# Kernel tuning notes

Hardware: AMD Instinct MI355X
Metric: run time of the kernel (lower is better)

## Reference

```python
import jax, jax.numpy as jnp
import numpy as np

D_MODEL = 2048
NUM_Q_HEADS = 16
NUM_KV_HEADS = 4
HEAD_DIM = D_MODEL // NUM_Q_HEADS  # 128
NUM_GROUPS = NUM_Q_HEADS // NUM_KV_HEADS  # 4
ROPE_BASE = 10000.0


def _rope_cos_sin(seq_len, head_dim):
    inv_freq = 1.0 / (ROPE_BASE ** (jnp.arange(0, head_dim, 2, dtype=jnp.float32) / head_dim))
    t = jnp.arange(seq_len, dtype=jnp.float32)
    freqs = jnp.outer(t, inv_freq)            # [S, head_dim/2]
    emb = jnp.concatenate([freqs, freqs], -1)  # [S, head_dim]
    return jnp.cos(emb)[None, :, None, :], jnp.sin(emb)[None, :, None, :]


def _rotate_half(x):
    half = x.shape[-1] // 2
    return jnp.concatenate([-x[..., half:], x[..., :half]], axis=-1)


def setup_inputs() -> dict:
    key = jax.random.key(0)
    k0, k1, k2, k3, k4 = jax.random.split(key, 5)
    B, S = 2, 2048
    kv_dim = HEAD_DIM * NUM_KV_HEADS
    scale = D_MODEL ** -0.5
    return {
        "x": jax.random.normal(k0, (B, S, D_MODEL), jnp.float32),
        "attention_mask": jnp.ones((B, S), jnp.int32),
        "Wq": jax.random.normal(k1, (D_MODEL, D_MODEL), jnp.float32) * scale,
        "Wk": jax.random.normal(k2, (D_MODEL, kv_dim), jnp.float32) * scale,
        "Wv": jax.random.normal(k3, (D_MODEL, kv_dim), jnp.float32) * scale,
        "Wo": jax.random.normal(k4, (D_MODEL, D_MODEL), jnp.float32) * scale,
    }


def reference(x, attention_mask, Wq, Wk, Wv, Wo):
    B, S, _ = x.shape
    q = (x @ Wq).reshape(B, S, NUM_Q_HEADS, HEAD_DIM)
    k = (x @ Wk).reshape(B, S, NUM_KV_HEADS, HEAD_DIM)
    v = (x @ Wv).reshape(B, S, NUM_KV_HEADS, HEAD_DIM)

    cos, sin = _rope_cos_sin(S, HEAD_DIM)  # [1,S,1,hd]
    q = q * cos + _rotate_half(q) * sin
    k = k * cos + _rotate_half(k) * sin

    # [B, H, S, hd]; replicate KV heads across groups (repeat_interleave)
    q = q.transpose(0, 2, 1, 3)
    k = jnp.repeat(k.transpose(0, 2, 1, 3), NUM_GROUPS, axis=1)
    v = jnp.repeat(v.transpose(0, 2, 1, 3), NUM_GROUPS, axis=1)

    scale = HEAD_DIM ** -0.5
    scores = jnp.einsum("bhqd,bhkd->bhqk", q, k) * scale
    mask = attention_mask[:, None, None, :]  # [B,1,1,S] over keys
    scores = jnp.where(mask == 0, jnp.float32(-jnp.inf), scores)
    probs = jax.nn.softmax(scores, axis=-1)
    out = jnp.einsum("bhqk,bhkd->bhqd", probs, v)
    out = out.transpose(0, 2, 1, 3).reshape(B, S, D_MODEL)
    return out @ Wo
```

## Files before the change

### kernel.cpp

```cpp
#include <hip/hip_runtime.h>
#include <hip/hip_bf16.h>

typedef __attribute__((ext_vector_type(4))) float f32x4;
typedef __attribute__((ext_vector_type(16))) float f32x16;
typedef __attribute__((ext_vector_type(8))) short s16x8;
typedef __attribute__((ext_vector_type(4))) short s16x4;
typedef __attribute__((ext_vector_type(2))) unsigned int u32x2;

__device__ __forceinline__ float fexp2(float x) {
    float y; asm("v_exp_f32 %0, %1" : "=v"(y) : "v"(x)); return y;
}

__global__ void tables_prep(float* __restrict__ cosT, float* __restrict__ sinT,
                            const int* __restrict__ mask, float* __restrict__ mb) {
    const int bid = blockIdx.x;
    if (bid < 2048) {
        const int s = bid, j = threadIdx.x;
        const float inv = exp2f(-(float)j * (13.287712379549449f / 64.f));
        const float f = (float)s * inv;
        cosT[s * 64 + j] = cosf(f);
        sinT[s * 64 + j] = sinf(f);
    } else {
        const int base = (bid - 2048) * 64 + threadIdx.x;
#pragma unroll
        for (int k = 0; k < 4; ++k)
            mb[base + k * 1024] = (mask[base + k * 1024] == 0) ? -1e30f : 0.f;
    }
}

__global__ __launch_bounds__(256)
void cast_f32_bf16(const float* __restrict__ src, __hip_bfloat16* __restrict__ dst, int n4) {
    const int i = blockIdx.x * 256 + threadIdx.x;
    if (i < n4) {
        f32x4 v = *reinterpret_cast<const f32x4*>(src + (size_t)i * 4);
        union { s16x4 v4; __hip_bfloat16 h[4]; } u;
#pragma unroll
        for (int j = 0; j < 4; ++j) u.h[j] = __float2bfloat16(v[j]);
        *reinterpret_cast<s16x4*>(dst + (size_t)i * 4) = u.v4;
    }
}

__global__ __launch_bounds__(256)
void transpose_cast_all(const float* __restrict__ Wq, const float* __restrict__ Wk,
                        const float* __restrict__ Wv, const float* __restrict__ Wo,
                        __hip_bfloat16* __restrict__ wqkv_t, __hip_bfloat16* __restrict__ wo_t) {
    __shared__ __align__(16) float t[32][33];
    const int tx = threadIdx.x, ty = threadIdx.y;
    const int xseg = blockIdx.x;
    const int r0 = blockIdx.y * 32;
    const float* src; __hip_bfloat16* dst; int C, c0;
    if (xseg < 64)      { src = Wq; dst = wqkv_t;                  C = 2048; c0 = xseg * 32; }
    else if (xseg < 80) { src = Wk; dst = wqkv_t + 2048ULL * 2048; C = 512;  c0 = (xseg - 64) * 32; }
    else if (xseg < 96) { src = Wv; dst = wqkv_t + 2560ULL * 2048; C = 512;  c0 = (xseg - 80) * 32; }
    else                { src = Wo; dst = wo_t;                    C = 2048; c0 = (xseg - 96) * 32; }
#pragma unroll
    for (int i = 0; i < 32; i += 8)
        t[ty + i][tx] = src[(size_t)(r0 + ty + i) * C + c0 + tx];
    __syncthreads();
#pragma unroll
    for (int i = 0; i < 32; i += 8)
        dst[(size_t)(c0 + ty + i) * 2048 + r0 + tx] = __float2bfloat16(t[tx][ty + i]);
}

__global__ __launch_bounds__(256)
void vt_transpose(const __hip_bfloat16* __restrict__ qkv, __hip_bfloat16* __restrict__ Vt) {
    __shared__ unsigned short t[32][33];
    const int tx = threadIdx.x, ty = threadIdx.y;
    const int s0 = blockIdx.x * 32, d0 = blockIdx.y * 32;
    const int bh = blockIdx.z, b = bh >> 2, hh = bh & 3;
    const unsigned short* q = (const unsigned short*)qkv;
#pragma unroll
    for (int i = 0; i < 32; i += 8)
        t[ty + i][tx] = q[(size_t)(b * 2048 + s0 + ty + i) * 3072 + 2560 + hh * 128 + d0 + tx];
    __syncthreads();
#pragma unroll
    for (int i = 0; i < 32; i += 8)
        ((unsigned short*)Vt)[((size_t)(bh * 128) + d0 + ty + i) * 2048 + s0 + tx] = t[tx][ty + i];
}

template<int NI, bool BF16OUT>
__global__ __launch_bounds__(512, 1)
void gemm256_bt(const __hip_bfloat16* __restrict__ A,
                const __hip_bfloat16* __restrict__ Bt,
                void* __restrict__ Cv, int M, int N, int K, int NX) {
    __shared__ __align__(16) __hip_bfloat16 sm[4][2][8192];
    const int tid = threadIdx.x;
    const int l = tid & 63, w = tid >> 6;
    const int lo = l & 15, hi = l >> 4;
    const int wm = w >> 2, wn = w & 3;
    const int id = blockIdx.x, slot = id >> 3;
    const int by = (id & 7) * 2 + slot / NX;
    const int bx = slot % NX;
    const int row0 = by * 256;
    const int col0 = bx * (NI * 64);
    const int nk = K >> 5;

    f32x4 acc[8][NI];
#pragma unroll
    for (int mi = 0; mi < 8; ++mi)
#pragma unroll
        for (int ni = 0; ni < NI; ++ni) acc[mi][ni] = f32x4{0.f, 0.f, 0.f, 0.f};

    auto ldlds = [&](const __hip_bfloat16* gsrc, __hip_bfloat16* ldst) {
        __builtin_amdgcn_global_load_lds(
            (const __attribute__((address_space(1))) void*)gsrc,
            (__attribute__((address_space(3))) void*)ldst, 16, 0, 0);
    };
    auto stage = [&](int kt) {
        const int s = kt & 3, k0 = kt << 5;
#pragma unroll
        for (int i = 0; i < 2; ++i) {
            const int c = i * 512 + tid;
            const int r = c >> 2, sw = ((c & 3) ^ ((r >> 1) & 3)) * 8;
            ldlds(A + (size_t)(row0 + r) * K + k0 + sw, &sm[s][0][c * 8]);
        }
        {
            const int c = tid;
            const int r = c >> 2, sw = ((c & 3) ^ ((r >> 1) & 3)) * 8;
            ldlds(Bt + (size_t)(col0 + r) * K + k0 + sw, &sm[s][1][c * 8]);
        }
        if constexpr (NI == 4) {
            const int c = 512 + tid;
            const int r = c >> 2, sw = ((c & 3) ^ ((r >> 1) & 3)) * 8;
            ldlds(Bt + (size_t)(col0 + r) * K + k0 + sw, &sm[s][1][c * 8]);
        } else if constexpr (NI == 3) {
            if (tid < 256) {
                const int c = 512 + tid;
                const int r = c >> 2, sw = ((c & 3) ^ ((r >> 1) & 3)) * 8;
                ldlds(Bt + (size_t)(col0 + r) * K + k0 + sw, &sm[s][1][c * 8]);
            }
        }
    };

    stage(0); stage(1); stage(2);
    for (int kt = 0; kt < nk; ++kt) {
        const int s = kt & 3;
        if (kt < nk - 2) {
            if constexpr (NI == 4)      asm volatile("s_waitcnt vmcnt(8)" ::: "memory");
            else if constexpr (NI == 2) asm volatile("s_waitcnt vmcnt(6)" ::: "memory");
            else { if (tid < 256) asm volatile("s_waitcnt vmcnt(8)" ::: "memory");
                   else           asm volatile("s_waitcnt vmcnt(6)" ::: "memory"); }
        } else if (kt == nk - 2) {
            if constexpr (NI == 4)      asm volatile("s_waitcnt vmcnt(4)" ::: "memory");
            else if constexpr (NI == 2) asm volatile("s_waitcnt vmcnt(3)" ::: "memory");
            else { if (tid < 256) asm volatile("s_waitcnt vmcnt(4)" ::: "memory");
                   else           asm volatile("s_waitcnt vmcnt(3)" ::: "memory"); }
        } else {
            asm volatile("s_waitcnt vmcnt(0)" ::: "memory");
        }
        asm volatile("s_waitcnt lgkmcnt(0)" ::: "memory");
        asm volatile("s_barrier" ::: "memory");
        if (kt + 3 < nk) stage(kt + 3);

        s16x8 af[8], bf[NI];
        const int rsw = ((lo >> 1) & 3);
#pragma unroll
        for (int mi = 0; mi < 8; ++mi)
            af[mi] = *reinterpret_cast<const s16x8*>(
                &sm[s][0][(wm * 128 + mi * 16 + lo) * 32 + ((hi ^ rsw) * 8)]);
#pragma unroll
        for (int ni = 0; ni < NI; ++ni)
            bf[ni] = *reinterpret_cast<const s16x8*>(
                &sm[s][1][(wn * NI * 16 + ni * 16 + lo) * 32 + ((hi ^ rsw) * 8)]);
        __builtin_amdgcn_s_setprio(1);
#pragma unroll
        for (int mi = 0; mi < 8; ++mi)
#pragma unroll
            for (int ni = 0; ni < NI; ++ni)
                acc[mi][ni] = __builtin_amdgcn_mfma_f32_16x16x32_bf16(af[mi], bf[ni], acc[mi][ni], 0, 0, 0);
        __builtin_amdgcn_s_setprio(0);
    }
    const int rbase = row0 + wm * 128 + hi * 4;
    const int cbase = col0 + wn * NI * 16 + lo;
    if constexpr (BF16OUT) {
        __hip_bfloat16* C = (__hip_bfloat16*)Cv;
#pragma unroll
        for (int mi = 0; mi < 8; ++mi)
#pragma unroll
            for (int ni = 0; ni < NI; ++ni)
#pragma unroll
                for (int r = 0; r < 4; ++r)
                    C[(size_t)(rbase + mi * 16 + r) * N + cbase + ni * 16] =
                        __float2bfloat16(acc[mi][ni][r]);
    } else {
        float* C = (float*)Cv;
#pragma unroll
        for (int mi = 0; mi < 8; ++mi)
#pragma unroll
            for (int ni = 0; ni < NI; ++ni)
#pragma unroll
                for (int r = 0; r < 4; ++r)
                    C[(size_t)(rbase + mi * 16 + r) * N + cbase + ni * 16] = acc[mi][ni][r];
    }
}

__global__ __launch_bounds__(512, 1)
void gemm128x256_bt(const __hip_bfloat16* __restrict__ A,
                    const __hip_bfloat16* __restrict__ Bt,
                    float* __restrict__ C, int M, int N, int K) {
    __shared__ __align__(16) __hip_bfloat16 smA[4][4096];
    __shared__ __align__(16) __hip_bfloat16 smB[4][8192];
    const int tid = threadIdx.x;
    const int l = tid & 63, w = tid >> 6;
    const int lo = l & 15, hi = l >> 4;
    const int wm = w >> 2, wn = w & 3;
    const int id = blockIdx.x, slot = id >> 3;
    const int by = (id & 7) * 4 + slot / 8;
    const int bx = slot % 8;
    const int row0 = by * 128;
    const int col0 = bx * 256;
    const int nk = K >> 5;

    f32x4 acc[4][4];
#pragma unroll
    for (int mi = 0; mi < 4; ++mi)
#pragma unroll
        for (int ni = 0; ni < 4; ++ni) acc[mi][ni] = f32x4{0.f, 0.f, 0.f, 0.f};

    auto ldlds = [&](const __hip_bfloat16* gsrc, __hip_bfloat16* ldst) {
        __builtin_amdgcn_global_load_lds(
            (const __attribute__((address_space(1))) void*)gsrc,
            (__attribute__((address_space(3))) void*)ldst, 16, 0, 0);
    };
    auto stage = [&](int kt) {
        const int s = kt & 3, k0 = kt << 5;
        {
            const int c = tid;
            const int r = c >> 2, sw = ((c & 3) ^ ((r >> 1) & 3)) * 8;
            ldlds(A + (size_t)(row0 + r) * K + k0 + sw, &smA[s][c * 8]);
        }
#pragma unroll
        for (int i = 0; i < 2; ++i) {
            const int c = i * 512 + tid;
            const int r = c >> 2, sw = ((c & 3) ^ ((r >> 1) & 3)) * 8;
            ldlds(Bt + (size_t)(col0 + r) * K + k0 + sw, &smB[s][c * 8]);
        }
    };

    stage(0); stage(1); stage(2);
    for (int kt = 0; kt < nk; ++kt) {
        const int s = kt & 3;
        if (kt < nk - 2)       asm volatile("s_waitcnt vmcnt(6)" ::: "memory");
        else if (kt == nk - 2) asm volatile("s_waitcnt vmcnt(3)" ::: "memory");
        else                   asm volatile("s_waitcnt vmcnt(0)" ::: "memory");
        asm volatile("s_waitcnt lgkmcnt(0)" ::: "memory");
        asm volatile("s_barrier" ::: "memory");
        if (kt + 3 < nk) stage(kt + 3);

        s16x8 af[4], bf[4];
        const int rsw = ((lo >> 1) & 3);
#pragma unroll
        for (int mi = 0; mi < 4; ++mi)
            af[mi] = *reinterpret_cast<const s16x8*>(
                &smA[s][(wm * 64 + mi * 16 + lo) * 32 + ((hi ^ rsw) * 8)]);
#pragma unroll
        for (int ni = 0; ni < 4; ++ni)
            bf[ni] = *reinterpret_cast<const s16x8*>(
                &smB[s][(wn * 64 + ni * 16 + lo) * 32 + ((hi ^ rsw) * 8)]);
        __builtin_amdgcn_s_setprio(1);
#pragma unroll
        for (int mi = 0; mi < 4; ++mi)
#pragma unroll
            for (int ni = 0; ni < 4; ++ni)
                acc[mi][ni] = __builtin_amdgcn_mfma_f32_16x16x32_bf16(af[mi], bf[ni], acc[mi][ni], 0, 0, 0);
        __builtin_amdgcn_s_setprio(0);
    }
    const int rbase = row0 + wm * 64 + hi * 4;
    const int cbase = col0 + wn * 64 + lo;
#pragma unroll
    for (int mi = 0; mi < 4; ++mi)
#pragma unroll
        for (int ni = 0; ni < 4; ++ni)
#pragma unroll
            for (int r = 0; r < 4; ++r)
                C[(size_t)(rbase + mi * 16 + r) * N + cbase + ni * 16] = acc[mi][ni][r];
}

__global__ __launch_bounds__(256)
void rope_scatter(const __hip_bfloat16* __restrict__ qkv,
                  const float* __restrict__ cosT, const float* __restrict__ sinT,
                  __hip_bfloat16* __restrict__ Qr, __hip_bfloat16* __restrict__ Kr) {
    const int m = blockIdx.y;
    const int col4 = blockIdx.x * 256 + threadIdx.x;
    if (col4 >= 640) return;
    const int col = col4 * 4;
    const int b = m >> 11, s = m & 2047;
    const int d = col & 127;
    const int j = d & 63;
    union { s16x4 v4; __hip_bfloat16 h[4]; } vv, pp, u;
    vv.v4 = *reinterpret_cast<const s16x4*>(qkv + (size_t)m * 3072 + col);
    pp.v4 = *reinterpret_cast<const s16x4*>(qkv + (size_t)m * 3072 + (col ^ 64));
    const f32x4 c4 = *reinterpret_cast<const f32x4*>(cosT + s * 64 + j);
    const f32x4 s4 = *reinterpret_cast<const f32x4*>(sinT + s * 64 + j);
    const float sgn = (d < 64) ? -1.f : 1.f;
#pragma unroll
    for (int i = 0; i < 4; ++i)
        u.h[i] = __float2bfloat16(__bfloat162float(vv.h[i]) * c4[i] +
                                  sgn * __bfloat162float(pp.h[i]) * s4[i]);
    if (col < 2048) {
        const int hh = col >> 7;
        *reinterpret_cast<s16x4*>(&Qr[((size_t)(b * 16 + hh) * 2048 + s) * 128 + d]) = u.v4;
    } else {
        const int hh = (col - 2048) >> 7;
        *reinterpret_cast<s16x4*>(&Kr[((size_t)(b * 4 + hh) * 2048 + s) * 128 + d]) = u.v4;
    }
}

__global__ __launch_bounds__(256, 2)
void attn_kernel(const __hip_bfloat16* __restrict__ Qr,
                 const __hip_bfloat16* __restrict__ Kr,
                 const __hip_bfloat16* __restrict__ Vt,
                 const float* __restrict__ maskb,
                 __hip_bfloat16* __restrict__ Oo) {
    const int S = 2048;
    const int id = blockIdx.x;
    const int v = (id & 7) * 64 + (id >> 3);
    const int qt = v & 15;
    const int bh = v >> 4;
    const int b = bh >> 4, h = bh & 15, kvh = h >> 2;
    const int tid = threadIdx.x;
    const int l = tid & 63, wv_ = tid >> 6;
    const int lq = l & 31, hi2 = l >> 5;
    __shared__ __align__(16) __hip_bfloat16 Ks[2][64 * 128];
    __shared__ __align__(16) __hip_bfloat16 Vs[2][128 * 64];

    const __hip_bfloat16* Qb = Qr + (size_t)(b * 16 + h) * S * 128;
    const __hip_bfloat16* Kb = Kr + (size_t)(b * 4 + kvh) * S * 128;
    const __hip_bfloat16* Vb = Vt + (size_t)(b * 4 + kvh) * 128 * S;
    const float* mrow = maskb + b * S;

    const int qrow = qt * 128 + wv_ * 32 + lq;
    s16x8 qf[8];
#pragma unroll
    for (int ks = 0; ks < 8; ++ks)
        qf[ks] = *reinterpret_cast<const s16x8*>(Qb + (size_t)qrow * 128 + ks * 16 + hi2 * 8);

    float m_run = 0.f, l_run = 0.f;
    f32x16 o[4];
#pragma unroll
    for (int dt = 0; dt < 4; ++dt)
#pragma unroll
        for (int r = 0; r < 16; ++r) o[dt][r] = 0.f;
    const float scale2 = 0.12751682f;

    const int krow = tid >> 4, kc8 = tid & 15;
    const int koff = (kc8 ^ (krow & 7)) * 8;
    const int vrow = tid >> 3, vc8 = tid & 7;
    const int voff = (vc8 ^ (vrow & 7)) * 8;

    s16x8 kreg[4], vreg[4];
    auto load_tile = [&](int kv0) {
#pragma unroll
        for (int i = 0; i < 4; ++i)
            kreg[i] = *reinterpret_cast<const s16x8*>(
                Kb + (size_t)(kv0 + i * 16 + krow) * 128 + kc8 * 8);
#pragma unroll
        for (int i = 0; i < 4; ++i)
            vreg[i] = *reinterpret_cast<const s16x8*>(
                Vb + (size_t)(i * 32 + vrow) * S + kv0 + vc8 * 8);
    };

    auto body = [&](int kt, __hip_bfloat16* Kc, __hip_bfloat16* Vc) {
        const int kv0 = kt * 64;
        f32x4 bi[2][4];
#pragma unroll
        for (int sub = 0; sub < 2; ++sub)
#pragma unroll
            for (int r4 = 0; r4 < 4; ++r4)
                bi[sub][r4] = *reinterpret_cast<const f32x4*>(
                    mrow + kv0 + sub * 32 + r4 * 8 + hi2 * 4);
#pragma unroll
        for (int i = 0; i < 4; ++i)
            *reinterpret_cast<s16x8*>(Kc + (i * 16 + krow) * 128 + koff) = kreg[i];
#pragma unroll
        for (int i = 0; i < 4; ++i)
            *reinterpret_cast<s16x8*>(Vc + (i * 32 + vrow) * 64 + voff) = vreg[i];
        if (kt < 31) load_tile(kv0 + 64);
        asm volatile("s_waitcnt lgkmcnt(0)" ::: "memory");
        asm volatile("s_barrier" ::: "memory");

        f32x16 sc[2];
#pragma unroll
        for (int sub = 0; sub < 2; ++sub)
#pragma unroll
            for (int r = 0; r < 16; ++r) sc[sub][r] = 0.f;
        __builtin_amdgcn_s_setprio(1);
#pragma unroll
        for (int sub = 0; sub < 2; ++sub) {
            const int kr = sub * 32 + lq;
            const int ksw = kr & 7;
#pragma unroll
            for (int ks = 0; ks < 8; ++ks) {
                s16x8 kf = *reinterpret_cast<const s16x8*>(
                    Kc + kr * 128 + (((ks * 2 + hi2) ^ ksw) * 8));
                sc[sub] = __builtin_amdgcn_mfma_f32_32x32x16_bf16(kf, qf[ks], sc[sub], 0, 0, 0);
            }
        }
        __builtin_amdgcn_s_setprio(0);
#pragma unroll
        for (int sub = 0; sub < 2; ++sub)
#pragma unroll
            for (int r = 0; r < 16; ++r)
                sc[sub][r] = fmaf(sc[sub][r], scale2, bi[sub][r >> 2][r & 3]);
        float mx = sc[0][0];
#pragma unroll
        for (int sub = 0; sub < 2; ++sub)
#pragma unroll
            for (int r = 0; r < 16; ++r) mx = fmaxf(mx, sc[sub][r]);
        float ss = 0.f;
#pragma unroll
        for (int sub = 0; sub < 2; ++sub)
#pragma unroll
            for (int r = 0; r < 16; ++r) {
                sc[sub][r] = fexp2(sc[sub][r] - m_run);
                ss += sc[sub][r];
            }
        mx = fmaxf(mx, __shfl_xor(mx, 32));
        if (__ballot(mx > m_run + 11.5417f) != 0ull) {
            const float mnew = fmaxf(m_run, mx);
            const float alpha = fexp2(m_run - mnew);
            m_run = mnew;
            l_run *= alpha;
            ss *= alpha;
#pragma unroll
            for (int sub = 0; sub < 2; ++sub)
#pragma unroll
                for (int r = 0; r < 16; ++r) sc[sub][r] *= alpha;
#pragma unroll
            for (int dt = 0; dt < 4; ++dt)
#pragma unroll
                for (int r = 0; r < 16; ++r) o[dt][r] *= alpha;
        }
        ss += __shfl_xor(ss, 32);
        l_run += ss;
        unsigned int wvp[8][2];
#pragma unroll
        for (int g = 0; g < 8; ++g) {
            const int sub = g >> 2, r4 = g & 3;
            asm("v_cvt_pk_bf16_f32 %0, %1, %2"
                : "=v"(wvp[g][0]) : "v"(sc[sub][r4 * 4 + 0]), "v"(sc[sub][r4 * 4 + 1]));
            asm("v_cvt_pk_bf16_f32 %0, %1, %2"
                : "=v"(wvp[g][1]) : "v"(sc[sub][r4 * 4 + 2]), "v"(sc[sub][r4 * 4 + 3]));
        }
        __builtin_amdgcn_s_setprio(1);
#pragma unroll
        for (int ks = 0; ks < 4; ++ks) {
            u32x2 r0 = __builtin_amdgcn_permlane32_swap(wvp[2 * ks][0], wvp[2 * ks + 1][0], false, false);
            u32x2 r1 = __builtin_amdgcn_permlane32_swap(wvp[2 * ks][1], wvp[2 * ks + 1][1], false, false);
            union { unsigned int u[4]; s16x8 v; } pf;
            pf.u[0] = r0.x; pf.u[1] = r1.x; pf.u[2] = r0.y; pf.u[3] = r1.y;
#pragma unroll
            for (int dt = 0; dt < 4; ++dt) {
                const int dvr = dt * 32 + lq;
                s16x8 vf = *reinterpret_cast<const s16x8*>(
                    Vc + dvr * 64 + (((ks * 2 + hi2) ^ (dvr & 7)) * 8));
                o[dt] = __builtin_amdgcn_mfma_f32_32x32x16_bf16(vf, pf.v, o[dt], 0, 0, 0);
            }
        }
        __builtin_amdgcn_s_setprio(0);
    };

    load_tile(0);
    for (int kt2 = 0; kt2 < 16; ++kt2) {
        body(2 * kt2,     &Ks[0][0], &Vs[0][0]);
        body(2 * kt2 + 1, &Ks[1][0], &Vs[1][0]);
    }
    const float inv = 1.f / l_run;
    const size_t obase = (size_t)(b * S + qt * 128 + wv_ * 32 + lq) * 2048 + h * 128;
#pragma unroll
    for (int dt = 0; dt < 4; ++dt)
#pragma unroll
        for (int r4 = 0; r4 < 4; ++r4) {
            union { s16x4 v4; __hip_bfloat16 hh[4]; } u;
#pragma unroll
            for (int j = 0; j < 4; ++j)
                u.hh[j] = __float2bfloat16(o[dt][r4 * 4 + j] * inv);
            *reinterpret_cast<s16x4*>(&Oo[obase + dt * 32 + r4 * 8 + hi2 * 4]) = u.v4;
        }
}

extern "C" void kernel_launch(void* const* d_in, const int* in_sizes, int n_in,
                              void* d_out, int out_size, void* d_ws, size_t ws_size,
                              hipStream_t stream) {
    const float* x  = (const float*)d_in[0];
    const int* mask = (const int*)d_in[1];
    const float* Wq = (const float*)d_in[2];
    const float* Wk = (const float*)d_in[3];
    const float* Wv = (const float*)d_in[4];
    const float* Wo = (const float*)d_in[5];
    float* out = (float*)d_out;

    char* ws = (char*)d_ws;
    size_t off = 0;
    auto alloc = [&](size_t bytes) -> void* {
        void* p = ws + off;
        off += (bytes + 255) & ~(size_t)255;
        return p;
    };
    __hip_bfloat16* xb     = (__hip_bfloat16*)alloc(4096ULL * 2048 * 2);
    __hip_bfloat16* wqkv_t = (__hip_bfloat16*)alloc(3072ULL * 2048 * 2);
    __hip_bfloat16* wo_t   = (__hip_bfloat16*)alloc(2048ULL * 2048 * 2);
    __hip_bfloat16* qkvb   = (__hip_bfloat16*)alloc(4096ULL * 3072 * 2);
    __hip_bfloat16* Kr     = (__hip_bfloat16*)alloc(2ULL * 4 * 2048 * 128 * 2);
    __hip_bfloat16* Vt     = (__hip_bfloat16*)alloc(2ULL * 4 * 2048 * 128 * 2);
    float*          cosT   = (float*)alloc(2048ULL * 64 * 4);
    float*          sinT   = (float*)alloc(2048ULL * 64 * 4);
    float*          maskb  = (float*)alloc(2ULL * 2048 * 4);
    __hip_bfloat16* attno  = (__hip_bfloat16*)alloc(4096ULL * 2048 * 2);
    __hip_bfloat16* Qr    = xb;

    tables_prep<<<dim3(2064), dim3(64), 0, stream>>>(cosT, sinT, mask, maskb);
    cast_f32_bf16<<<dim3(8192), dim3(256), 0, stream>>>(x, xb, 2097152);
    transpose_cast_all<<<dim3(160, 64), dim3(32, 8), 0, stream>>>(Wq, Wk, Wv, Wo, wqkv_t, wo_t);

    gemm256_bt<3, true><<<dim3(256), dim3(512), 0, stream>>>(xb, wqkv_t, qkvb, 4096, 3072, 2048, 16);
    rope_scatter<<<dim3(3, 4096), dim3(256), 0, stream>>>(qkvb, cosT, sinT, Qr, Kr);
    vt_transpose<<<dim3(64, 4, 8), dim3(32, 8), 0, stream>>>(qkvb, Vt);
    attn_kernel<<<dim3(512), dim3(256), 0, stream>>>(Qr, Kr, Vt, maskb, attno);
    gemm128x256_bt<<<dim3(256), dim3(512), 0, stream>>>(attno, wo_t, out, 4096, 2048, 2048);
}
```

Before: 231.1 us.

## Fuse RoPE and V transpose into QKV GEMM epilogue with permuted weight rows

Permutes the Q/K weight rows during the transpose-cast so each wave holds matching rotate-half column pairs in registers. The QKV GEMM epilogue can then apply RoPE and write Q, K directly in head-major layout and V transposed. This removes the intermediate qkv buffer and the separate rope_scatter and vt_transpose kernels. It also changes the cos/sin tables to a position-contiguous layout and switches the output projection to the 256-row GEMM with NI=2, at the cost of scattered, uncoalesced epilogue stores and a 192-block grid on 256 CUs.

```diff
diff --git a/kernel.cpp b/kernel.cpp
--- a/kernel.cpp
+++ b/kernel.cpp
@@ -11,20 +11,22 @@
     float y; asm("v_exp_f32 %0, %1" : "=v"(y) : "v"(x)); return y;
 }
 
-__global__ void tables_prep(float* __restrict__ cosT, float* __restrict__ sinT,
+__global__ void tables_prep(float* __restrict__ cosT2, float* __restrict__ sinT2,
                             const int* __restrict__ mask, float* __restrict__ mb) {
     const int bid = blockIdx.x;
-    if (bid < 2048) {
-        const int s = bid, j = threadIdx.x;
+    if (bid < 64) {
+        const int j = bid;
         const float inv = exp2f(-(float)j * (13.287712379549449f / 64.f));
-        const float f = (float)s * inv;
-        cosT[s * 64 + j] = cosf(f);
-        sinT[s * 64 + j] = sinf(f);
+#pragma unroll
+        for (int k = 0; k < 8; ++k) {
+            const int s = k * 256 + threadIdx.x;
+            const float f = (float)s * inv;
+            cosT2[j * 2048 + s] = cosf(f);
+            sinT2[j * 2048 + s] = sinf(f);
+        }
     } else {
-        const int base = (bid - 2048) * 64 + threadIdx.x;
-#pragma unroll
-        for (int k = 0; k < 4; ++k)
-            mb[base + k * 1024] = (mask[base + k * 1024] == 0) ? -1e30f : 0.f;
+        const int idx = (bid - 64) * 256 + threadIdx.x;
+        mb[idx] = (mask[idx] == 0) ? -1e30f : 0.f;
     }
 }
 
@@ -48,34 +50,145 @@
     const int tx = threadIdx.x, ty = threadIdx.y;
     const int xseg = blockIdx.x;
     const int r0 = blockIdx.y * 32;
-    const float* src; __hip_bfloat16* dst; int C, c0;
-    if (xseg < 64)      { src = Wq; dst = wqkv_t;                  C = 2048; c0 = xseg * 32; }
-    else if (xseg < 80) { src = Wk; dst = wqkv_t + 2048ULL * 2048; C = 512;  c0 = (xseg - 64) * 32; }
-    else if (xseg < 96) { src = Wv; dst = wqkv_t + 2560ULL * 2048; C = 512;  c0 = (xseg - 80) * 32; }
-    else                { src = Wo; dst = wo_t;                    C = 2048; c0 = (xseg - 96) * 32; }
+    const float* src; __hip_bfloat16* dst; int C, c0; bool perm;
+    if (xseg < 64)      { src = Wq; dst = wqkv_t;                  C = 2048; c0 = xseg * 32;        perm = true; }
+    else if (xseg < 80) { src = Wk; dst = wqkv_t + 2048ULL * 2048; C = 512;  c0 = (xseg - 64) * 32; perm = true; }
+    else if (xseg < 96) { src = Wv; dst = wqkv_t + 2560ULL * 2048; C = 512;  c0 = (xseg - 80) * 32; perm = false; }
+    else                { src = Wo; dst = wo_t;                    C = 2048; c0 = (xseg - 96) * 32; perm = false; }
 #pragma unroll
     for (int i = 0; i < 32; i += 8)
         t[ty + i][tx] = src[(size_t)(r0 + ty + i) * C + c0 + tx];
     __syncthreads();
 #pragma unroll
-    for (int i = 0; i < 32; i += 8)
-        dst[(size_t)(c0 + ty + i) * 2048 + r0 + tx] = __float2bfloat16(t[tx][ty + i]);
-}
-
-__global__ __launch_bounds__(256)
-void vt_transpose(const __hip_bfloat16* __restrict__ qkv, __hip_bfloat16* __restrict__ Vt) {
-    __shared__ unsigned short t[32][33];
-    const int tx = threadIdx.x, ty = threadIdx.y;
-    const int s0 = blockIdx.x * 32, d0 = blockIdx.y * 32;
-    const int bh = blockIdx.z, b = bh >> 2, hh = bh & 3;
-    const unsigned short* q = (const unsigned short*)qkv;
-#pragma unroll
-    for (int i = 0; i < 32; i += 8)
-        t[ty + i][tx] = q[(size_t)(b * 2048 + s0 + ty + i) * 3072 + 2560 + hh * 128 + d0 + tx];
-    __syncthreads();
-#pragma unroll
-    for (int i = 0; i < 32; i += 8)
-        ((unsigned short*)Vt)[((size_t)(bh * 128) + d0 + ty + i) * 2048 + s0 + tx] = t[tx][ty + i];
+    for (int i = 0; i < 32; i += 8) {
+        int row = c0 + ty + i;
+        if (perm)
+            row = (row & ~127) + (row & 15) + 32 * ((row >> 4) & 3) + 16 * ((row >> 6) & 1);
+        dst[(size_t)row * 2048 + r0 + tx] = __float2bfloat16(t[tx][ty + i]);
+    }
+}
+
+__global__ __launch_bounds__(512, 1)
+void gemm_qkv_fused(const __hip_bfloat16* __restrict__ A,
+                    const __hip_bfloat16* __restrict__ Bt,
+                    const float* __restrict__ cosT2, const float* __restrict__ sinT2,
+                    __hip_bfloat16* __restrict__ Qr, __hip_bfloat16* __restrict__ Kr,
+                    __hip_bfloat16* __restrict__ Vt, int K) {
+    __shared__ __align__(16) __hip_bfloat16 sm[4][2][8192];
+    const int tid = threadIdx.x;
+    const int l = tid & 63, w = tid >> 6;
+    const int lo = l & 15, hi = l >> 4;
+    const int wm = w >> 2, wn = w & 3;
+    const int id = blockIdx.x, slot = id >> 3;
+    const int by = (id & 7) * 2 + slot / 12;
+    const int bx = slot % 12;
+    const int row0 = by * 256;
+    const int col0 = bx * 256;
+    const int nk = K >> 5;
+
+    f32x4 acc[8][4];
+#pragma unroll
+    for (int mi = 0; mi < 8; ++mi)
+#pragma unroll
+        for (int ni = 0; ni < 4; ++ni) acc[mi][ni] = f32x4{0.f, 0.f, 0.f, 0.f};
+
+    auto ldlds = [&](const __hip_bfloat16* gsrc, __hip_bfloat16* ldst) {
+        __builtin_amdgcn_global_load_lds(
+            (const __attribute__((address_space(1))) void*)gsrc,
+            (__attribute__((address_space(3))) void*)ldst, 16, 0, 0);
+    };
+    auto stage = [&](int kt) {
+        const int s = kt & 3, k0 = kt << 5;
+#pragma unroll
+        for (int i = 0; i < 2; ++i) {
+            const int c = i * 512 + tid;
+            const int r = c >> 2, sw = ((c & 3) ^ ((r >> 1) & 3)) * 8;
+            ldlds(A + (size_t)(row0 + r) * K + k0 + sw, &sm[s][0][c * 8]);
+        }
+#pragma unroll
+        for (int i = 0; i < 2; ++i) {
+            const int c = i * 512 + tid;
+            const int r = c >> 2, sw = ((c & 3) ^ ((r >> 1) & 3)) * 8;
+            ldlds(Bt + (size_t)(col0 + r) * K + k0 + sw, &sm[s][1][c * 8]);
+        }
+    };
+
+    stage(0); stage(1); stage(2);
+    for (int kt = 0; kt < nk; ++kt) {
+        const int s = kt & 3;
+        if (kt < nk - 2)       asm volatile("s_waitcnt vmcnt(8)" ::: "memory");
+        else if (kt == nk - 2) asm volatile("s_waitcnt vmcnt(4)" ::: "memory");
+        else                   asm volatile("s_waitcnt vmcnt(0)" ::: "memory");
+        asm volatile("s_waitcnt lgkmcnt(0)" ::: "memory");
+        asm volatile("s_barrier" ::: "memory");
+        if (kt + 3 < nk) stage(kt + 3);
+
+        s16x8 af[8], bf[4];
+        const int rsw = ((lo >> 1) & 3);
+#pragma unroll
+        for (int mi = 0; mi < 8; ++mi)
+            af[mi] = *reinterpret_cast<const s16x8*>(
+                &sm[s][0][(wm * 128 + mi * 16 + lo) * 32 + ((hi ^ rsw) * 8)]);
+#pragma unroll
+        for (int ni = 0; ni < 4; ++ni)
+            bf[ni] = *reinterpret_cast<const s16x8*>(
+                &sm[s][1][(wn * 64 + ni * 16 + lo) * 32 + ((hi ^ rsw) * 8)]);
+        __builtin_amdgcn_s_setprio(1);
+#pragma unroll
+        for (int mi = 0; mi < 8; ++mi)
+#pragma unroll
+            for (int ni = 0; ni < 4; ++ni)
+                acc[mi][ni] = __builtin_amdgcn_mfma_f32_16x16x32_bf16(af[mi], bf[ni], acc[mi][ni], 0, 0, 0);
+        __builtin_amdgcn_s_setprio(0);
+    }
+
+    const int rbase = row0 + wm * 128 + hi * 4;
+    if (bx < 10) {
+        const int cw = col0 + wn * 64;
+        const bool isQ = (bx < 8);
+        const int head = (isQ ? cw : cw - 2048) >> 7;
+        __hip_bfloat16* dst = isQ ? (Qr + ((size_t)head * 2048) * 128)
+                                  : (Kr + ((size_t)head * 2048) * 128);
+        const size_t bstride = (isQ ? 16ull : 4ull) * 2048 * 128;
+        const int jbase = 32 * (wn & 1) + lo;
+#pragma unroll
+        for (int mi = 0; mi < 8; ++mi) {
+            const int tok = rbase + mi * 16;
+            const int b = tok >> 11, s0 = tok & 2047;
+            __hip_bfloat16* drow = dst + b * bstride + (size_t)s0 * 128;
+#pragma unroll
+            for (int np = 0; np < 2; ++np) {
+                const int j = jbase + 16 * np;
+                const f32x4 c4 = *reinterpret_cast<const f32x4*>(cosT2 + j * 2048 + s0);
+                const f32x4 s4 = *reinterpret_cast<const f32x4*>(sinT2 + j * 2048 + s0);
+                const int ni0 = 2 * np, ni1 = 2 * np + 1;
+                const int dd0 = j;
+#pragma unroll
+                for (int r = 0; r < 4; ++r) {
+                    const float v0 = acc[mi][ni0][r], v1 = acc[mi][ni1][r];
+                    drow[(size_t)r * 128 + dd0]      = __float2bfloat16(v0 * c4[r] - v1 * s4[r]);
+                    drow[(size_t)r * 128 + dd0 + 64] = __float2bfloat16(v1 * c4[r] + v0 * s4[r]);
+                }
+            }
+        }
+    } else {
+        const int cw = col0 + wn * 64 - 2560;
+        const int hh = cw >> 7;
+#pragma unroll
+        for (int mi = 0; mi < 8; ++mi) {
+            const int tok = rbase + mi * 16;
+            const int b = tok >> 11, s0 = tok & 2047;
+#pragma unroll
+            for (int ni = 0; ni < 4; ++ni) {
+                const int dd = (cw & 127) + ni * 16 + lo;
+                union { s16x4 v4; __hip_bfloat16 h[4]; } u;
+#pragma unroll
+                for (int r = 0; r < 4; ++r) u.h[r] = __float2bfloat16(acc[mi][ni][r]);
+                *reinterpret_cast<s16x4*>(
+                    &Vt[((size_t)(b * 4 + hh) * 128 + dd) * 2048 + s0]) = u.v4;
+            }
+        }
+    }
 }
 
 template<int NI, bool BF16OUT>
@@ -123,12 +236,6 @@
             const int c = 512 + tid;
             const int r = c >> 2, sw = ((c & 3) ^ ((r >> 1) & 3)) * 8;
             ldlds(Bt + (size_t)(col0 + r) * K + k0 + sw, &sm[s][1][c * 8]);
-        } else if constexpr (NI == 3) {
-            if (tid < 256) {
-                const int c = 512 + tid;
-                const int r = c >> 2, sw = ((c & 3) ^ ((r >> 1) & 3)) * 8;
-                ldlds(Bt + (size_t)(col0 + r) * K + k0 + sw, &sm[s][1][c * 8]);
-            }
         }
     };
 
@@ -136,15 +243,11 @@
     for (int kt = 0; kt < nk; ++kt) {
         const int s = kt & 3;
         if (kt < nk - 2) {
-            if constexpr (NI == 4)      asm volatile("s_waitcnt vmcnt(8)" ::: "memory");
-            else if constexpr (NI == 2) asm volatile("s_waitcnt vmcnt(6)" ::: "memory");
-            else { if (tid < 256) asm volatile("s_waitcnt vmcnt(8)" ::: "memory");
-                   else           asm volatile("s_waitcnt vmcnt(6)" ::: "memory"); }
+            if constexpr (NI == 4) asm volatile("s_waitcnt vmcnt(8)" ::: "memory");
+            else                   asm volatile("s_waitcnt vmcnt(6)" ::: "memory");
         } else if (kt == nk - 2) {
-            if constexpr (NI == 4)      asm volatile("s_waitcnt vmcnt(4)" ::: "memory");
-            else if constexpr (NI == 2) asm volatile("s_waitcnt vmcnt(3)" ::: "memory");
-            else { if (tid < 256) asm volatile("s_waitcnt vmcnt(4)" ::: "memory");
-                   else           asm volatile("s_waitcnt vmcnt(3)" ::: "memory"); }
+            if constexpr (NI == 4) asm volatile("s_waitcnt vmcnt(4)" ::: "memory");
+            else                   asm volatile("s_waitcnt vmcnt(3)" ::: "memory");
         } else {
             asm volatile("s_waitcnt vmcnt(0)" ::: "memory");
         }
@@ -191,118 +294,6 @@
 #pragma unroll
                 for (int r = 0; r < 4; ++r)
                     C[(size_t)(rbase + mi * 16 + r) * N + cbase + ni * 16] = acc[mi][ni][r];
-    }
-}
-
-__global__ __launch_bounds__(512, 1)
-void gemm128x256_bt(const __hip_bfloat16* __restrict__ A,
-                    const __hip_bfloat16* __restrict__ Bt,
-                    float* __restrict__ C, int M, int N, int K) {
-    __shared__ __align__(16) __hip_bfloat16 smA[4][4096];
-    __shared__ __align__(16) __hip_bfloat16 smB[4][8192];
-    const int tid = threadIdx.x;
-    const int l = tid & 63, w = tid >> 6;
-    const int lo = l & 15, hi = l >> 4;
-    const int wm = w >> 2, wn = w & 3;
-    const int id = blockIdx.x, slot = id >> 3;
-    const int by = (id & 7) * 4 + slot / 8;
-    const int bx = slot % 8;
-    const int row0 = by * 128;
-    const int col0 = bx * 256;
-    const int nk = K >> 5;
-
-    f32x4 acc[4][4];
-#pragma unroll
-    for (int mi = 0; mi < 4; ++mi)
-#pragma unroll
-        for (int ni = 0; ni < 4; ++ni) acc[mi][ni] = f32x4{0.f, 0.f, 0.f, 0.f};
-
-    auto ldlds = [&](const __hip_bfloat16* gsrc, __hip_bfloat16* ldst) {
-        __builtin_amdgcn_global_load_lds(
-            (const __attribute__((address_space(1))) void*)gsrc,
-            (__attribute__((address_space(3))) void*)ldst, 16, 0, 0);
-    };
-    auto stage = [&](int kt) {
-        const int s = kt & 3, k0 = kt << 5;
-        {
-            const int c = tid;
-            const int r = c >> 2, sw = ((c & 3) ^ ((r >> 1) & 3)) * 8;
-            ldlds(A + (size_t)(row0 + r) * K + k0 + sw, &smA[s][c * 8]);
-        }
-#pragma unroll
-        for (int i = 0; i < 2; ++i) {
-            const int c = i * 512 + tid;
-            const int r = c >> 2, sw = ((c & 3) ^ ((r >> 1) & 3)) * 8;
-            ldlds(Bt + (size_t)(col0 + r) * K + k0 + sw, &smB[s][c * 8]);
-        }
-    };
-
-    stage(0); stage(1); stage(2);
-    for (int kt = 0; kt < nk; ++kt) {
-        const int s = kt & 3;
-        if (kt < nk - 2)       asm volatile("s_waitcnt vmcnt(6)" ::: "memory");
-        else if (kt == nk - 2) asm volatile("s_waitcnt vmcnt(3)" ::: "memory");
-        else                   asm volatile("s_waitcnt vmcnt(0)" ::: "memory");
-        asm volatile("s_waitcnt lgkmcnt(0)" ::: "memory");
-        asm volatile("s_barrier" ::: "memory");
-        if (kt + 3 < nk) stage(kt + 3);
-
-        s16x8 af[4], bf[4];
-        const int rsw = ((lo >> 1) & 3);
-#pragma unroll
-        for (int mi = 0; mi < 4; ++mi)
-            af[mi] = *reinterpret_cast<const s16x8*>(
-                &smA[s][(wm * 64 + mi * 16 + lo) * 32 + ((hi ^ rsw) * 8)]);
-#pragma unroll
-        for (int ni = 0; ni < 4; ++ni)
-            bf[ni] = *reinterpret_cast<const s16x8*>(
-                &smB[s][(wn * 64 + ni * 16 + lo) * 32 + ((hi ^ rsw) * 8)]);
-        __builtin_amdgcn_s_setprio(1);
-#pragma unroll
-        for (int mi = 0; mi < 4; ++mi)
-#pragma unroll
-            for (int ni = 0; ni < 4; ++ni)
-                acc[mi][ni] = __builtin_amdgcn_mfma_f32_16x16x32_bf16(af[mi], bf[ni], acc[mi][ni], 0, 0, 0);
-        __builtin_amdgcn_s_setprio(0);
-    }
-    const int rbase = row0 + wm * 64 + hi * 4;
-    const int cbase = col0 + wn * 64 + lo;
-#pragma unroll
-    for (int mi = 0; mi < 4; ++mi)
-#pragma unroll
-        for (int ni = 0; ni < 4; ++ni)
-#pragma unroll
-            for (int r = 0; r < 4; ++r)
-                C[(size_t)(rbase + mi * 16 + r) * N + cbase + ni * 16] = acc[mi][ni][r];
-}
-
-__global__ __launch_bounds__(256)
-void rope_scatter(const __hip_bfloat16* __restrict__ qkv,
-                  const float* __restrict__ cosT, const float* __restrict__ sinT,
-                  __hip_bfloat16* __restrict__ Qr, __hip_bfloat16* __restrict__ Kr) {
-    const int m = blockIdx.y;
-    const int col4 = blockIdx.x * 256 + threadIdx.x;
-    if (col4 >= 640) return;
-    const int col = col4 * 4;
-    const int b = m >> 11, s = m & 2047;
-    const int d = col & 127;
-    const int j = d & 63;
-    union { s16x4 v4; __hip_bfloat16 h[4]; } vv, pp, u;
-    vv.v4 = *reinterpret_cast<const s16x4*>(qkv + (size_t)m * 3072 + col);
-    pp.v4 = *reinterpret_cast<const s16x4*>(qkv + (size_t)m * 3072 + (col ^ 64));
-    const f32x4 c4 = *reinterpret_cast<const f32x4*>(cosT + s * 64 + j);
-    const f32x4 s4 = *reinterpret_cast<const f32x4*>(sinT + s * 64 + j);
-    const float sgn = (d < 64) ? -1.f : 1.f;
-#pragma unroll
-    for (int i = 0; i < 4; ++i)
-        u.h[i] = __float2bfloat16(__bfloat162float(vv.h[i]) * c4[i] +
-                                  sgn * __bfloat162float(pp.h[i]) * s4[i]);
-    if (col < 2048) {
-        const int hh = col >> 7;
-        *reinterpret_cast<s16x4*>(&Qr[((size_t)(b * 16 + hh) * 2048 + s) * 128 + d]) = u.v4;
-    } else {
-        const int hh = (col - 2048) >> 7;
-        *reinterpret_cast<s16x4*>(&Kr[((size_t)(b * 4 + hh) * 2048 + s) * 128 + d]) = u.v4;
     }
 }
 
@@ -500,22 +491,20 @@
     __hip_bfloat16* xb     = (__hip_bfloat16*)alloc(4096ULL * 2048 * 2);
     __hip_bfloat16* wqkv_t = (__hip_bfloat16*)alloc(3072ULL * 2048 * 2);
     __hip_bfloat16* wo_t   = (__hip_bfloat16*)alloc(2048ULL * 2048 * 2);
-    __hip_bfloat16* qkvb   = (__hip_bfloat16*)alloc(4096ULL * 3072 * 2);
+    __hip_bfloat16* Qr     = (__hip_bfloat16*)alloc(2ULL * 16 * 2048 * 128 * 2);
     __hip_bfloat16* Kr     = (__hip_bfloat16*)alloc(2ULL * 4 * 2048 * 128 * 2);
     __hip_bfloat16* Vt     = (__hip_bfloat16*)alloc(2ULL * 4 * 2048 * 128 * 2);
-    float*          cosT   = (float*)alloc(2048ULL * 64 * 4);
-    float*          sinT   = (float*)alloc(2048ULL * 64 * 4);
+    float*          cosT2  = (float*)alloc(64ULL * 2048 * 4);
+    float*          sinT2  = (float*)alloc(64ULL * 2048 * 4);
     float*          maskb  = (float*)alloc(2ULL * 2048 * 4);
     __hip_bfloat16* attno  = (__hip_bfloat16*)alloc(4096ULL * 2048 * 2);
-    __hip_bfloat16* Qr    = xb;
-
-    tables_prep<<<dim3(2064), dim3(64), 0, stream>>>(cosT, sinT, mask, maskb);
+
+    tables_prep<<<dim3(80), dim3(256), 0, stream>>>(cosT2, sinT2, mask, maskb);
     cast_f32_bf16<<<dim3(8192), dim3(256), 0, stream>>>(x, xb, 2097152);
     transpose_cast_all<<<dim3(160, 64), dim3(32, 8), 0, stream>>>(Wq, Wk, Wv, Wo, wqkv_t, wo_t);
 
-    gemm256_bt<3, true><<<dim3(256), dim3(512), 0, stream>>>(xb, wqkv_t, qkvb, 4096, 3072, 2048, 16);
-    rope_scatter<<<dim3(3, 4096), dim3(256), 0, stream>>>(qkvb, cosT, sinT, Qr, Kr);
-    vt_transpose<<<dim3(64, 4, 8), dim3(32, 8), 0, stream>>>(qkvb, Vt);
+    gemm_qkv_fused<<<dim3(192), dim3(512), 0, stream>>>(xb, wqkv_t, cosT2, sinT2,
+                                                        Qr, Kr, Vt, 2048);
     attn_kernel<<<dim3(512), dim3(256), 0, stream>>>(Qr, Kr, Vt, maskb, attno);
-    gemm128x256_bt<<<dim3(256), dim3(512), 0, stream>>>(attno, wo_t, out, 4096, 2048, 2048);
-}
+    gemm256_bt<2, false><<<dim3(256), dim3(512), 0, stream>>>(attno, wo_t, out, 4096, 2048, 2048, 16);
+}
```

Result: faster. 211.3 us (-8.6%).
